# Kernel optimization log

Measured on AMD Instinct MI355X. Metric: run time of the kernel, lower is better.

The kernel has to match this reference:

```python
import jax, jax.numpy as jnp
import numpy as np

TEMPERATURE = 8.0
WINDOW_SIZE = 256
NEG = -1e9

def setup_inputs() -> dict:
    key = jax.random.key(0)
    kq, kk, kv = jax.random.split(key, 3)
    B, H, S, D = 2, 16, 2048, 64
    q = jax.random.normal(kq, (B, H, S, D), dtype=jnp.float32)
    k = jax.random.normal(kk, (B, H, S, D), dtype=jnp.float32)
    v = jax.random.normal(kv, (B, H, S, D), dtype=jnp.float32)
    return {"q": q, "k": k, "v": v}

def _window_mask(len_q, len_k, window_size):
    # causal + sliding window: position i attends to j in [i-window+1, i]
    i = jnp.arange(len_q)[:, None]
    j = jnp.arange(len_k)[None, :]
    allowed = (j <= i) & (j > i - window_size)
    return allowed  # [len_q, len_k] bool

def reference(q, k, v):
    B, H, Sq, D = q.shape
    Sk = k.shape[2]
    attn = jnp.einsum('bhqd,bhkd->bhqk', q, k) / TEMPERATURE
    allowed = _window_mask(Sq, Sk, WINDOW_SIZE)  # window_size < len_k path
    attn = jnp.where(allowed[None, None], attn, NEG)
    attn = jax.nn.softmax(attn, axis=-1)  # dropout is identity in eval
    out = jnp.einsum('bhqk,bhkd->bhqd', attn, v)
    return (out, attn)
```

## Files before the change

kernel.cpp:

```cpp
#include <hip/hip_runtime.h>


#define S_LEN 2048
#define DHEAD 64
#define TQ 32
#define UEXT 288
#define KV_STRIDE 72
#define SC_STRIDE 292

typedef float     f4v __attribute__((ext_vector_type(4)));
typedef _Float16  h2v __attribute__((ext_vector_type(2)));
typedef _Float16  h4v __attribute__((ext_vector_type(4)));

__device__ __forceinline__ float dot2f(float aBits, float bBits, float c) {
#if __has_builtin(__builtin_amdgcn_fdot2)
  return __builtin_amdgcn_fdot2(__builtin_bit_cast(h2v, aBits),
                                __builtin_bit_cast(h2v, bBits), c, false);
#else
  h2v a = __builtin_bit_cast(h2v, aBits);
  h2v b = __builtin_bit_cast(h2v, bBits);
  return c + (float)a.x * (float)b.x + (float)a.y * (float)b.y;
#endif
}

__global__ __launch_bounds__(512, 4)
void cwa_kernel(const float* __restrict__ q, const float* __restrict__ k,
                const float* __restrict__ v, float* __restrict__ out,
                float* __restrict__ attn)
{
  __shared__ __align__(16) _Float16 kv[UEXT][KV_STRIDE];
  __shared__ __align__(16) _Float16 kq[TQ][DHEAD];
  __shared__ __align__(16) _Float16 sc[TQ][SC_STRIDE];
  __shared__ float rinv[TQ];

  const int t    = threadIdx.x;
  const int lane = t & 63;
  const int wv   = t >> 6;
  const int trow = lane >> 4;
  const int tcol = lane & 15;

  const int blk   = ((blockIdx.x & 7) << 8) + (blockIdx.x >> 3);
  const int bh    = blk >> 6;
  const int i0    = (blk & 63) * TQ;
  const int jbase = i0 - 256;

  const size_t base = (size_t)bh * (S_LEN * DHEAD);
  const float* qb = q + base;
  const float* kb = k + base;
  const float* vb = v + base;

  const f4v fzero = {0.f, 0.f, 0.f, 0.f};

  {
    const int r = t >> 4, d4 = t & 15;
    f4v f = *(const f4v*)(qb + (size_t)(i0 + r) * DHEAD + 4 * d4);
    h4v h = { (_Float16)f.x, (_Float16)f.y, (_Float16)f.z, (_Float16)f.w };
    *(h4v*)&kq[r][4 * d4] = h;
  }
  #pragma unroll 3
  for (int w = 0; w < 9; ++w) {
    const int idx = t + 512 * w;
    const int u = idx >> 4, d4 = idx & 15;
    const int j = jbase + u;
    f4v f = fzero;
    if (j >= 0 && j < S_LEN) f = *(const f4v*)(kb + (size_t)j * DHEAD + 4 * d4);
    h4v h = { (_Float16)f.x, (_Float16)f.y, (_Float16)f.z, (_Float16)f.w };
    *(h4v*)&kv[u][4 * d4] = h;
  }
  __syncthreads();

  {
    const int r = 4 * wv + trow;
    f4v qreg[8];
    #pragma unroll
    for (int x = 0; x < 8; ++x) qreg[x] = *(const f4v*)&kq[r][8 * x];

    float rs = 0.f;
    #pragma unroll 3
    for (int j18 = 0; j18 < 18; ++j18) {
      const int u = tcol + 16 * j18;
      float a = 0.f;
      #pragma unroll
      for (int x = 0; x < 8; ++x) {
        const f4v kr = *(const f4v*)&kv[u][8 * x];
        a = dot2f(qreg[x].x, kr.x, a);
        a = dot2f(qreg[x].y, kr.y, a);
        a = dot2f(qreg[x].z, kr.z, a);
        a = dot2f(qreg[x].w, kr.w, a);
      }
      const bool valid = (u >= r + 1) && (u <= r + 256) && (u >= 256 - i0);
      const float p = valid ? __expf(a * 0.125f) : 0.f;
      sc[r][u] = (_Float16)p;
      rs += p;
    }
    if (tcol < 4) sc[r][288 + tcol] = (_Float16)0.f;
    #pragma unroll
    for (int off = 8; off; off >>= 1) rs += __shfl_down(rs, off, 64);
    if (tcol == 0) rinv[r] = 1.f / rs;
  }
  __syncthreads();

  #pragma unroll 3
  for (int w = 0; w < 9; ++w) {
    const int idx = t + 512 * w;
    const int u = idx >> 4, d4 = idx & 15;
    const int j = jbase + u;
    f4v f = fzero;
    if (j >= 0 && j < S_LEN) f = *(const f4v*)(vb + (size_t)j * DHEAD + 4 * d4);
    h4v h = { (_Float16)f.x, (_Float16)f.y, (_Float16)f.z, (_Float16)f.w };
    *(h4v*)&kv[u][4 * d4] = h;
  }
  __syncthreads();

  float* abase = attn + (size_t)(bh * S_LEN + i0) * S_LEN;
  const int er  = t >> 4;
  const int eir = i0 + er;
  int glo = (eir - 255) >> 2;  if (glo < 0) glo = 0;
  const int ghi = eir >> 2;
  float* erow = abase + (size_t)er * S_LEN;

  #pragma unroll 8
  for (int w = 0; w < 32; ++w) {
    const int u4 = tcol + 16 * w;
    if (u4 < glo || u4 > ghi)
      __builtin_nontemporal_store(fzero, (f4v*)(erow + 4 * u4));
  }

  {
    const float inv = rinv[er];
    #pragma unroll
    for (int w = 0; w < 5; ++w) {
      const int u4 = glo + tcol + 16 * w;
      if (u4 <= ghi) {
        const int u0 = 4 * u4 - jbase;
        h4v ph = *(const h4v*)&sc[er][u0];
        f4v val = { (float)ph.x * inv, (float)ph.y * inv,
                    (float)ph.z * inv, (float)ph.w * inv };
        __builtin_nontemporal_store(val, (f4v*)(erow + 4 * u4));
      }
    }
  }

  {
    f4v acc[4];
    #pragma unroll
    for (int i = 0; i < 4; ++i) acc[i] = fzero;
    const int u0 = 72 * trow;

    for (int s = 0; s < 18; ++s) {
      const int ub = u0 + 4 * s;
      h4v ph[4], vh[4];
      #pragma unroll
      for (int i = 0; i < 4; ++i) ph[i] = *(const h4v*)&sc[4 * wv + i][ub];
      #pragma unroll
      for (int e = 0; e < 4; ++e) vh[e] = *(const h4v*)&kv[ub + e][4 * tcol];
      #pragma unroll
      for (int e = 0; e < 4; ++e) {
        const f4v vv = { (float)vh[e].x, (float)vh[e].y,
                         (float)vh[e].z, (float)vh[e].w };
        #pragma unroll
        for (int i = 0; i < 4; ++i) {
          const float p = (float)ph[i][e];
          acc[i].x = fmaf(p, vv.x, acc[i].x);
          acc[i].y = fmaf(p, vv.y, acc[i].y);
          acc[i].z = fmaf(p, vv.z, acc[i].z);
          acc[i].w = fmaf(p, vv.w, acc[i].w);
        }
      }
    }
    #pragma unroll
    for (int i = 0; i < 4; ++i) {
      #pragma unroll
      for (int c = 0; c < 4; ++c) {
        float x = acc[i][c];
        x += __shfl_down(x, 32, 64);
        x += __shfl_down(x, 16, 64);
        acc[i][c] = x;
      }
    }
    if (trow == 0) {
      #pragma unroll
      for (int i = 0; i < 4; ++i) {
        const int r = 4 * wv + i;
        const float inv = rinv[r];
        f4v o = { acc[i].x * inv, acc[i].y * inv,
                  acc[i].z * inv, acc[i].w * inv };
        __builtin_nontemporal_store(o,
            (f4v*)(out + (size_t)(bh * S_LEN + i0 + r) * DHEAD + 4 * tcol));
      }
    }
  }
}

extern "C" void kernel_launch(void* const* d_in, const int* in_sizes, int n_in,
                              void* d_out, int out_size, void* d_ws, size_t ws_size,
                              hipStream_t stream) {
  const float* q = (const float*)d_in[0];
  const float* k = (const float*)d_in[1];
  const float* v = (const float*)d_in[2];
  float* out  = (float*)d_out;
  float* attn = out + (size_t)2 * 16 * 2048 * 64;

  dim3 grid(2048), block(512);
  hipLaunchKernelGGL(cwa_kernel, grid, block, 0, stream, q, k, v, out, attn);
}
```

Baseline: 612.7 us.

## Use MFMA for QK and PV, load K/V directly from global, 256-thread blocks

Replaces the packed-half dot-product QK^T and scalar-FMA PV loops with 16x16x32 f16 MFMA instructions. K and V are no longer staged in shared memory; each wave reads its fragments straight from global memory and converts them to half in registers. The block shrinks to 256 threads, and row sums are combined through a small per-wave buffer. The attn-matrix write path is kept but split into two passes. The risk is that the V loads are scalar and strided, which could make the memory traffic more scattered even though LDS use and one barrier are removed.

```diff
diff --git a/kernel.cpp b/kernel.cpp
--- a/kernel.cpp
+++ b/kernel.cpp
@@ -4,40 +4,37 @@
 #define S_LEN 2048
 #define DHEAD 64
 #define TQ 32
-#define UEXT 288
-#define KV_STRIDE 72
-#define SC_STRIDE 292
+#define NTC 18
+#define SC_STRIDE 296
 
-typedef float     f4v __attribute__((ext_vector_type(4)));
-typedef _Float16  h2v __attribute__((ext_vector_type(2)));
-typedef _Float16  h4v __attribute__((ext_vector_type(4)));
+typedef float    f4v __attribute__((ext_vector_type(4)));
+typedef _Float16 h4v __attribute__((ext_vector_type(4)));
+typedef _Float16 h8v __attribute__((ext_vector_type(8)));
 
-__device__ __forceinline__ float dot2f(float aBits, float bBits, float c) {
-#if __has_builtin(__builtin_amdgcn_fdot2)
-  return __builtin_amdgcn_fdot2(__builtin_bit_cast(h2v, aBits),
-                                __builtin_bit_cast(h2v, bBits), c, false);
-#else
-  h2v a = __builtin_bit_cast(h2v, aBits);
-  h2v b = __builtin_bit_cast(h2v, bBits);
-  return c + (float)a.x * (float)b.x + (float)a.y * (float)b.y;
-#endif
+__device__ __forceinline__ h8v load8h(const float* p) {
+  f4v a = *(const f4v*)p;
+  f4v b = *(const f4v*)(p + 4);
+  h8v h;
+  h[0] = (_Float16)a.x; h[1] = (_Float16)a.y;
+  h[2] = (_Float16)a.z; h[3] = (_Float16)a.w;
+  h[4] = (_Float16)b.x; h[5] = (_Float16)b.y;
+  h[6] = (_Float16)b.z; h[7] = (_Float16)b.w;
+  return h;
 }
 
-__global__ __launch_bounds__(512, 4)
+__global__ __launch_bounds__(256, 4)
 void cwa_kernel(const float* __restrict__ q, const float* __restrict__ k,
                 const float* __restrict__ v, float* __restrict__ out,
                 float* __restrict__ attn)
 {
-  __shared__ __align__(16) _Float16 kv[UEXT][KV_STRIDE];
-  __shared__ __align__(16) _Float16 kq[TQ][DHEAD];
   __shared__ __align__(16) _Float16 sc[TQ][SC_STRIDE];
-  __shared__ float rinv[TQ];
+  __shared__ float rsp[4][16];
 
-  const int t    = threadIdx.x;
+  const int t  = threadIdx.x;
   const int lane = t & 63;
-  const int wv   = t >> 6;
-  const int trow = lane >> 4;
-  const int tcol = lane & 15;
+  const int wv = t >> 6;
+  const int g  = lane >> 4;
+  const int nl = lane & 15;
 
   const int blk   = ((blockIdx.x & 7) << 8) + (blockIdx.x >> 3);
   const int bh    = blk >> 6;
@@ -52,82 +49,106 @@
   const f4v fzero = {0.f, 0.f, 0.f, 0.f};
 
   {
-    const int r = t >> 4, d4 = t & 15;
-    f4v f = *(const f4v*)(qb + (size_t)(i0 + r) * DHEAD + 4 * d4);
-    h4v h = { (_Float16)f.x, (_Float16)f.y, (_Float16)f.z, (_Float16)f.w };
-    *(h4v*)&kq[r][4 * d4] = h;
-  }
-  #pragma unroll 3
-  for (int w = 0; w < 9; ++w) {
-    const int idx = t + 512 * w;
-    const int u = idx >> 4, d4 = idx & 15;
-    const int j = jbase + u;
-    f4v f = fzero;
-    if (j >= 0 && j < S_LEN) f = *(const f4v*)(kb + (size_t)j * DHEAD + 4 * d4);
-    h4v h = { (_Float16)f.x, (_Float16)f.y, (_Float16)f.z, (_Float16)f.w };
-    *(h4v*)&kv[u][4 * d4] = h;
+    const int tr = wv >> 1;
+    const int qrow = i0 + tr * 16 + nl;
+    h8v qf0 = load8h(qb + (size_t)qrow * DHEAD + 8 * g);
+    h8v qf1 = load8h(qb + (size_t)qrow * DHEAD + 32 + 8 * g);
+
+    float rs0 = 0.f, rs1 = 0.f, rs2 = 0.f, rs3 = 0.f;
+    const int tcsub = wv & 1;
+
+    #pragma unroll 3
+    for (int kk = 0; kk < 9; ++kk) {
+      const int tc = tcsub + 2 * kk;
+      int j = jbase + tc * 16 + nl;
+      j = j < 0 ? 0 : j;
+      const float* krow = kb + (size_t)j * DHEAD;
+      h8v kf0 = load8h(krow + 8 * g);
+      h8v kf1 = load8h(krow + 32 + 8 * g);
+      f4v acc = fzero;
+      acc = __builtin_amdgcn_mfma_f32_16x16x32_f16(qf0, kf0, acc, 0, 0, 0);
+      acc = __builtin_amdgcn_mfma_f32_16x16x32_f16(qf1, kf1, acc, 0, 0, 0);
+
+      #pragma unroll
+      for (int jj = 0; jj < 4; ++jj) {
+        const int r = tr * 16 + 4 * g + jj;
+        const int u = tc * 16 + nl;
+        const bool valid = (u >= r + 1) && (u <= r + 256) && (u >= 256 - i0);
+        const float p = valid ? __expf(acc[jj] * 0.125f) : 0.f;
+        sc[r][u] = (_Float16)p;
+        if (jj == 0) rs0 += p; else if (jj == 1) rs1 += p;
+        else if (jj == 2) rs2 += p; else rs3 += p;
+      }
+    }
+    #pragma unroll
+    for (int off = 8; off; off >>= 1) {
+      rs0 += __shfl_down(rs0, off, 64);
+      rs1 += __shfl_down(rs1, off, 64);
+      rs2 += __shfl_down(rs2, off, 64);
+      rs3 += __shfl_down(rs3, off, 64);
+    }
+    if (nl == 0) {
+      rsp[wv][4 * g + 0] = rs0;
+      rsp[wv][4 * g + 1] = rs1;
+      rsp[wv][4 * g + 2] = rs2;
+      rsp[wv][4 * g + 3] = rs3;
+    }
   }
   __syncthreads();
 
   {
-    const int r = 4 * wv + trow;
-    f4v qreg[8];
+    const int tr2 = wv >> 1;
+    const int nc0 = (wv & 1) * 2;
+    f4v pa0 = fzero, pa1 = fzero;
+
+    #pragma unroll 2
+    for (int kk = 0; kk < 9; ++kk) {
+      const int kb0 = 32 * kk;
+      h8v pf = *(const h8v*)&sc[tr2 * 16 + nl][kb0 + 8 * g];
+      const int u0 = kb0 + 8 * g;
+      h8v vf0, vf1;
+      #pragma unroll
+      for (int e = 0; e < 8; ++e) {
+        int j = jbase + u0 + e;
+        j = j < 0 ? 0 : j;
+        const float* vrow = vb + (size_t)j * DHEAD + nl;
+        vf0[e] = (_Float16)vrow[nc0 * 16];
+        vf1[e] = (_Float16)vrow[nc0 * 16 + 16];
+      }
+      pa0 = __builtin_amdgcn_mfma_f32_16x16x32_f16(pf, vf0, pa0, 0, 0, 0);
+      pa1 = __builtin_amdgcn_mfma_f32_16x16x32_f16(pf, vf1, pa1, 0, 0, 0);
+    }
+
     #pragma unroll
-    for (int x = 0; x < 8; ++x) qreg[x] = *(const f4v*)&kq[r][8 * x];
-
-    float rs = 0.f;
-    #pragma unroll 3
-    for (int j18 = 0; j18 < 18; ++j18) {
-      const int u = tcol + 16 * j18;
-      float a = 0.f;
-      #pragma unroll
-      for (int x = 0; x < 8; ++x) {
-        const f4v kr = *(const f4v*)&kv[u][8 * x];
-        a = dot2f(qreg[x].x, kr.x, a);
-        a = dot2f(qreg[x].y, kr.y, a);
-        a = dot2f(qreg[x].z, kr.z, a);
-        a = dot2f(qreg[x].w, kr.w, a);
-      }
-      const bool valid = (u >= r + 1) && (u <= r + 256) && (u >= 256 - i0);
-      const float p = valid ? __expf(a * 0.125f) : 0.f;
-      sc[r][u] = (_Float16)p;
-      rs += p;
+    for (int jj = 0; jj < 4; ++jj) {
+      const int x = 4 * g + jj;
+      const float inv = 1.f / (rsp[2 * tr2][x] + rsp[2 * tr2 + 1][x]);
+      const int row = i0 + tr2 * 16 + x;
+      float* orow = out + (size_t)(bh * S_LEN + row) * DHEAD + nl;
+      __builtin_nontemporal_store(pa0[jj] * inv, orow + nc0 * 16);
+      __builtin_nontemporal_store(pa1[jj] * inv, orow + nc0 * 16 + 16);
     }
-    if (tcol < 4) sc[r][288 + tcol] = (_Float16)0.f;
-    #pragma unroll
-    for (int off = 8; off; off >>= 1) rs += __shfl_down(rs, off, 64);
-    if (tcol == 0) rinv[r] = 1.f / rs;
   }
-  __syncthreads();
-
-  #pragma unroll 3
-  for (int w = 0; w < 9; ++w) {
-    const int idx = t + 512 * w;
-    const int u = idx >> 4, d4 = idx & 15;
-    const int j = jbase + u;
-    f4v f = fzero;
-    if (j >= 0 && j < S_LEN) f = *(const f4v*)(vb + (size_t)j * DHEAD + 4 * d4);
-    h4v h = { (_Float16)f.x, (_Float16)f.y, (_Float16)f.z, (_Float16)f.w };
-    *(h4v*)&kv[u][4 * d4] = h;
-  }
-  __syncthreads();
 
   float* abase = attn + (size_t)(bh * S_LEN + i0) * S_LEN;
-  const int er  = t >> 4;
-  const int eir = i0 + er;
-  int glo = (eir - 255) >> 2;  if (glo < 0) glo = 0;
-  const int ghi = eir >> 2;
-  float* erow = abase + (size_t)er * S_LEN;
+  const int tcol = t & 15;
 
-  #pragma unroll 8
-  for (int w = 0; w < 32; ++w) {
-    const int u4 = tcol + 16 * w;
-    if (u4 < glo || u4 > ghi)
-      __builtin_nontemporal_store(fzero, (f4v*)(erow + 4 * u4));
-  }
+  #pragma unroll
+  for (int pass = 0; pass < 2; ++pass) {
+    const int er  = (t >> 4) + 16 * pass;
+    const int eir = i0 + er;
+    int glo = (eir - 255) >> 2;  if (glo < 0) glo = 0;
+    const int ghi = eir >> 2;
+    float* erow = abase + (size_t)er * S_LEN;
 
-  {
-    const float inv = rinv[er];
+    #pragma unroll 8
+    for (int w = 0; w < 32; ++w) {
+      const int u4 = tcol + 16 * w;
+      if (u4 < glo || u4 > ghi)
+        __builtin_nontemporal_store(fzero, (f4v*)(erow + 4 * u4));
+    }
+    const float inv = 1.f / (rsp[2 * (er >> 4)][er & 15] +
+                             rsp[2 * (er >> 4) + 1][er & 15]);
     #pragma unroll
     for (int w = 0; w < 5; ++w) {
       const int u4 = glo + tcol + 16 * w;
@@ -137,56 +158,6 @@
         f4v val = { (float)ph.x * inv, (float)ph.y * inv,
                     (float)ph.z * inv, (float)ph.w * inv };
         __builtin_nontemporal_store(val, (f4v*)(erow + 4 * u4));
-      }
-    }
-  }
-
-  {
-    f4v acc[4];
-    #pragma unroll
-    for (int i = 0; i < 4; ++i) acc[i] = fzero;
-    const int u0 = 72 * trow;
-
-    for (int s = 0; s < 18; ++s) {
-      const int ub = u0 + 4 * s;
-      h4v ph[4], vh[4];
-      #pragma unroll
-      for (int i = 0; i < 4; ++i) ph[i] = *(const h4v*)&sc[4 * wv + i][ub];
-      #pragma unroll
-      for (int e = 0; e < 4; ++e) vh[e] = *(const h4v*)&kv[ub + e][4 * tcol];
-      #pragma unroll
-      for (int e = 0; e < 4; ++e) {
-        const f4v vv = { (float)vh[e].x, (float)vh[e].y,
-                         (float)vh[e].z, (float)vh[e].w };
-        #pragma unroll
-        for (int i = 0; i < 4; ++i) {
-          const float p = (float)ph[i][e];
-          acc[i].x = fmaf(p, vv.x, acc[i].x);
-          acc[i].y = fmaf(p, vv.y, acc[i].y);
-          acc[i].z = fmaf(p, vv.z, acc[i].z);
-          acc[i].w = fmaf(p, vv.w, acc[i].w);
-        }
-      }
-    }
-    #pragma unroll
-    for (int i = 0; i < 4; ++i) {
-      #pragma unroll
-      for (int c = 0; c < 4; ++c) {
-        float x = acc[i][c];
-        x += __shfl_down(x, 32, 64);
-        x += __shfl_down(x, 16, 64);
-        acc[i][c] = x;
-      }
-    }
-    if (trow == 0) {
-      #pragma unroll
-      for (int i = 0; i < 4; ++i) {
-        const int r = 4 * wv + i;
-        const float inv = rinv[r];
-        f4v o = { acc[i].x * inv, acc[i].y * inv,
-                  acc[i].z * inv, acc[i].w * inv };
-        __builtin_nontemporal_store(o,
-            (f4v*)(out + (size_t)(bh * S_LEN + i0 + r) * DHEAD + 4 * tcol));
       }
     }
   }
@@ -201,6 +172,6 @@
   float* out  = (float*)d_out;
   float* attn = out + (size_t)2 * 16 * 2048 * 64;
 
-  dim3 grid(2048), block(512);
+  dim3 grid(2048), block(256);
   hipLaunchKernelGGL(cwa_kernel, grid, block, 0, stream, q, k, v, out, attn);
 }
```

New measurement: 609.1 us. About the same (-0.6%).
